# Kernel optimization log

Measured on AMD Instinct MI355X. Metric: run time of the kernel, lower is better.

The kernel has to match this reference:

```python
import jax, jax.numpy as jnp
import numpy as np

B, N, D = 16, 8192, 768
H = int(D * 4.0)  # mlp hidden
EPS = 1e-6
D_SQRT = D ** (-0.5)


def setup_inputs() -> dict:
    key = jax.random.key(0)
    ks = jax.random.split(key, 6)
    x = jax.random.normal(ks[0], (B, N, D), dtype=jnp.float32)
    # learnable query, trunc-normal std = D**-0.5 (plain normal is fine for a reference)
    query = jax.random.normal(ks[1], (D,), dtype=jnp.float32) * D_SQRT
    ln_gamma = jnp.ones((D,), dtype=jnp.float32)
    ln_beta = jnp.zeros((D,), dtype=jnp.float32)
    w1 = jax.random.normal(ks[2], (D, H), dtype=jnp.float32) * (D ** -0.5)
    b1 = jnp.zeros((H,), dtype=jnp.float32)
    w2 = jax.random.normal(ks[3], (H, D), dtype=jnp.float32) * (H ** -0.5)
    b2 = jnp.zeros((D,), dtype=jnp.float32)
    return {"x": x, "query": query, "ln_gamma": ln_gamma, "ln_beta": ln_beta,
            "w1": w1, "b1": b1, "w2": w2, "b2": b2}


def _layernorm(x, gamma, beta):
    mu = jnp.mean(x, axis=-1, keepdims=True)
    var = jnp.mean(jnp.square(x - mu), axis=-1, keepdims=True)
    return (x - mu) * jax.lax.rsqrt(var + EPS) * gamma + beta


def reference(x, query, ln_gamma, ln_beta, w1, b1, w2, b2):
    # single-query cross attention: attn [B, N]
    attn = jnp.einsum('d,bnd->bn', query, x)
    attn_sm = jax.nn.softmax(attn * D_SQRT, axis=-1)
    pooled = jnp.einsum('bn,bnd->bd', attn_sm, x)  # [B, D]
    h = _layernorm(pooled, ln_gamma, ln_beta)
    h = jax.nn.gelu(h @ w1 + b1, approximate=False) @ w2 + b2
    out = pooled + h
    return out, attn
```

## Files before the change

### kernel.cpp

```cpp
#include <hip/hip_runtime.h>
#include <hip/hip_bf16.h>
#include <math.h>

#define BB 16
#define NN 8192
#define DD 768
#define HH 3072
#define EPSV 1e-6f
#define DSQRT 0.03608439182435161f

#define CHUNKS 128
#define ROWS_PER_BLOCK (NN / CHUNKS)
#define NWAVES 4
#define ROWS_PER_WAVE (ROWS_PER_BLOCK / NWAVES)
#define PSTRIDE 772

#define KS1 16
#define KL1 (DD / KS1)
#define KS2 48
#define KL2 (HH / KS2)

__global__ __launch_bounds__(256, 4) void attn_pool_k(
    const float* __restrict__ x, const float* __restrict__ query,
    float* __restrict__ attn_out, float* __restrict__ partials)
{
    const int b     = blockIdx.y;
    const int chunk = blockIdx.x;
    const int tid   = threadIdx.x;
    const int wave  = tid >> 6;
    const int lane  = tid & 63;

    const float4* q4 = (const float4*)query;
    const float4 q0 = q4[lane];
    const float4 q1 = q4[lane + 64];
    const float4 q2 = q4[lane + 128];

    float4 p0 = make_float4(0.f, 0.f, 0.f, 0.f);
    float4 p1 = make_float4(0.f, 0.f, 0.f, 0.f);
    float4 p2 = make_float4(0.f, 0.f, 0.f, 0.f);
    float esum = 0.f;

    const int n0 = chunk * ROWS_PER_BLOCK + wave * ROWS_PER_WAVE;
    const float4* xb = (const float4*)(x + (size_t)b * NN * DD);

    #pragma unroll 2
    for (int r = 0; r < ROWS_PER_WAVE; ++r) {
        const int n = n0 + r;
        const float4* xr = xb + (size_t)n * (DD / 4);
        const float4 v0 = xr[lane];
        const float4 v1 = xr[lane + 64];
        const float4 v2 = xr[lane + 128];

        float s = v0.x * q0.x + v0.y * q0.y + v0.z * q0.z + v0.w * q0.w;
        s += v1.x * q1.x + v1.y * q1.y + v1.z * q1.z + v1.w * q1.w;
        s += v2.x * q2.x + v2.y * q2.y + v2.z * q2.z + v2.w * q2.w;
        #pragma unroll
        for (int off = 32; off > 0; off >>= 1) s += __shfl_xor(s, off);

        if (lane == 0) attn_out[(size_t)b * NN + n] = s;

        const float e = expf(s * DSQRT);
        esum += e;
        p0.x += e * v0.x; p0.y += e * v0.y; p0.z += e * v0.z; p0.w += e * v0.w;
        p1.x += e * v1.x; p1.y += e * v1.y; p1.z += e * v1.z; p1.w += e * v1.w;
        p2.x += e * v2.x; p2.y += e * v2.y; p2.z += e * v2.z; p2.w += e * v2.w;
    }

    __shared__ float lds[NWAVES][PSTRIDE];
    float* my = lds[wave];
    *(float4*)&my[lane * 4]       = p0;
    *(float4*)&my[256 + lane * 4] = p1;
    *(float4*)&my[512 + lane * 4] = p2;
    if (lane == 0) my[768] = esum;
    __syncthreads();

    float* outp = partials + (size_t)(b * CHUNKS + chunk) * PSTRIDE;
    #pragma unroll
    for (int k = 0; k < 3; ++k) {
        const int idx = tid + k * 256;
        outp[idx] = lds[0][idx] + lds[1][idx] + lds[2][idx] + lds[3][idx];
    }
    if (tid == 0) outp[768] = lds[0][768] + lds[1][768] + lds[2][768] + lds[3][768];
}

__global__ __launch_bounds__(768) void reduce_ln_k(
    const float* __restrict__ partials, const float* __restrict__ gamma,
    const float* __restrict__ beta, float* __restrict__ pooled_ws,
    float* __restrict__ hln_ws)
{
    const int b = blockIdx.x, tid = threadIdx.x;
    const float* pb = partials + (size_t)b * CHUNKS * PSTRIDE;

    float v = 0.f;
    #pragma unroll 8
    for (int c = 0; c < CHUNKS; ++c) v += pb[c * PSTRIDE + tid];

    __shared__ float s_den;
    if (tid < 64) {
        float dn = pb[tid * PSTRIDE + 768] + pb[(tid + 64) * PSTRIDE + 768];
        #pragma unroll
        for (int off = 32; off > 0; off >>= 1) dn += __shfl_xor(dn, off);
        if (tid == 0) s_den = dn;
    }
    __syncthreads();
    v *= (1.f / s_den);

    __shared__ float red[768];
    red[tid] = v;
    __syncthreads();
    if (tid < 256) red[tid] += red[tid + 256] + red[tid + 512];
    __syncthreads();
    for (int s = 128; s > 0; s >>= 1) {
        if (tid < s) red[tid] += red[tid + s];
        __syncthreads();
    }
    const float mu = red[0] * (1.f / 768.f);
    __syncthreads();

    const float dmu = v - mu;
    red[tid] = dmu * dmu;
    __syncthreads();
    if (tid < 256) red[tid] += red[tid + 256] + red[tid + 512];
    __syncthreads();
    for (int s = 128; s > 0; s >>= 1) {
        if (tid < s) red[tid] += red[tid + s];
        __syncthreads();
    }
    const float var = red[0] * (1.f / 768.f);
    const float rstd = rsqrtf(var + EPSV);

    pooled_ws[(size_t)b * DD + tid] = v;
    hln_ws[(size_t)b * DD + tid] = (v - mu) * rstd * gamma[tid] + beta[tid];
}

__global__ __launch_bounds__(256) void gemm1_part_k(
    const float* __restrict__ hln_ws, const float* __restrict__ w1,
    float* __restrict__ g1p)
{
    const int j  = blockIdx.x * 256 + threadIdx.x;
    const int k0 = blockIdx.y * KL1;

    __shared__ float hl[BB][KL1];
    for (int i = threadIdx.x; i < BB * KL1; i += 256) {
        const int b = i / KL1, d = i - b * KL1;
        hl[b][d] = hln_ws[(size_t)b * DD + k0 + d];
    }
    __syncthreads();

    float wv[KL1];
    #pragma unroll
    for (int d = 0; d < KL1; ++d) wv[d] = w1[(size_t)(k0 + d) * HH + j];

    float acc[BB];
    #pragma unroll
    for (int b = 0; b < BB; ++b) acc[b] = 0.f;

    #pragma unroll
    for (int d4 = 0; d4 < KL1 / 4; ++d4) {
        #pragma unroll
        for (int b = 0; b < BB; ++b) {
            const float4 h4 = *(const float4*)&hl[b][d4 * 4];
            acc[b] += h4.x * wv[d4 * 4] + h4.y * wv[d4 * 4 + 1]
                    + h4.z * wv[d4 * 4 + 2] + h4.w * wv[d4 * 4 + 3];
        }
    }

    float* op = g1p + (size_t)blockIdx.y * BB * HH;
    #pragma unroll
    for (int b = 0; b < BB; ++b) op[(size_t)b * HH + j] = acc[b];
}

__global__ __launch_bounds__(256) void comb1_gelu_k(
    const float* __restrict__ g1p, const float* __restrict__ b1,
    float* __restrict__ h1_ws)
{
    const int i = blockIdx.x * 256 + threadIdx.x;
    const int j = i % HH;

    float a = b1[j];
    #pragma unroll
    for (int s = 0; s < KS1; ++s) a += g1p[(size_t)s * BB * HH + i];
    h1_ws[i] = 0.5f * a * (1.f + erff(a * 0.70710678118654752f));
}

__global__ __launch_bounds__(256) void gemm2_part_k(
    const float* __restrict__ h1_ws, const float* __restrict__ w2,
    float* __restrict__ g2p)
{
    const int col = blockIdx.x * 256 + threadIdx.x;
    const int k0  = blockIdx.y * KL2;

    __shared__ float hg[BB][KL2];
    for (int i = threadIdx.x; i < BB * KL2; i += 256) {
        const int b = i / KL2, d = i - b * KL2;
        hg[b][d] = h1_ws[(size_t)b * HH + k0 + d];
    }
    __syncthreads();

    float wv[KL2];
    #pragma unroll
    for (int d = 0; d < KL2; ++d) wv[d] = w2[(size_t)(k0 + d) * DD + col];

    float acc[BB];
    #pragma unroll
    for (int b = 0; b < BB; ++b) acc[b] = 0.f;

    #pragma unroll
    for (int d4 = 0; d4 < KL2 / 4; ++d4) {
        #pragma unroll
        for (int b = 0; b < BB; ++b) {
            const float4 h4 = *(const float4*)&hg[b][d4 * 4];
            acc[b] += h4.x * wv[d4 * 4] + h4.y * wv[d4 * 4 + 1]
                    + h4.z * wv[d4 * 4 + 2] + h4.w * wv[d4 * 4 + 3];
        }
    }

    float* op = g2p + (size_t)blockIdx.y * BB * DD;
    #pragma unroll
    for (int b = 0; b < BB; ++b) op[(size_t)b * DD + col] = acc[b];
}

__global__ __launch_bounds__(256) void comb2_fin_k(
    const float* __restrict__ g2p, const float* __restrict__ pooled_ws,
    const float* __restrict__ b2, float* __restrict__ out)
{
    const int i = blockIdx.x * 256 + threadIdx.x;
    const int d = i % DD;

    float a = pooled_ws[i] + b2[d];
    #pragma unroll
    for (int s = 0; s < KS2; ++s) a += g2p[(size_t)s * BB * DD + i];
    out[i] = a;
}

extern "C" void kernel_launch(void* const* d_in, const int* in_sizes, int n_in,
                              void* d_out, int out_size, void* d_ws, size_t ws_size,
                              hipStream_t stream)
{
    const float* x     = (const float*)d_in[0];
    const float* query = (const float*)d_in[1];
    const float* gamma = (const float*)d_in[2];
    const float* beta  = (const float*)d_in[3];
    const float* w1    = (const float*)d_in[4];
    const float* b1    = (const float*)d_in[5];
    const float* w2    = (const float*)d_in[6];
    const float* b2    = (const float*)d_in[7];

    float* out      = (float*)d_out;
    float* attn_out = out + BB * DD;

    float* ws       = (float*)d_ws;
    float* partials = ws;
    float* pooled   = partials + BB * CHUNKS * PSTRIDE;
    float* hln      = pooled + BB * DD;
    float* h1       = hln + BB * DD;
    float* g1p      = h1 + BB * HH;
    float* g2p      = g1p + KS1 * BB * HH;

    attn_pool_k<<<dim3(CHUNKS, BB), 256, 0, stream>>>(x, query, attn_out, partials);
    reduce_ln_k<<<dim3(BB), 768, 0, stream>>>(partials, gamma, beta, pooled, hln);
    gemm1_part_k<<<dim3(HH / 256, KS1), 256, 0, stream>>>(hln, w1, g1p);
    comb1_gelu_k<<<dim3(BB * HH / 256), 256, 0, stream>>>(g1p, b1, h1);
    gemm2_part_k<<<dim3(DD / 256, KS2), 256, 0, stream>>>(h1, w2, g2p);
    comb2_fin_k<<<dim3(BB * DD / 256), 256, 0, stream>>>(g2p, pooled, b2, out);
}
```

Baseline: 119.5 us.

## Halve attention chunks and add parallel two-stage partial reduction

After: 109.6 us. 1.09x faster.

```diff
diff --git a/kernel.cpp b/kernel.cpp
--- a/kernel.cpp
+++ b/kernel.cpp
@@ -9,18 +9,19 @@
 #define EPSV 1e-6f
 #define DSQRT 0.03608439182435161f
 
-#define CHUNKS 128
+#define CHUNKS 64
 #define ROWS_PER_BLOCK (NN / CHUNKS)
 #define NWAVES 4
 #define ROWS_PER_WAVE (ROWS_PER_BLOCK / NWAVES)
 #define PSTRIDE 772
+#define QQ 4
 
 #define KS1 16
 #define KL1 (DD / KS1)
 #define KS2 48
 #define KL2 (HH / KS2)
 
-__global__ __launch_bounds__(256, 4) void attn_pool_k(
+__global__ __launch_bounds__(256) void attn_pool_k(
     const float* __restrict__ x, const float* __restrict__ query,
     float* __restrict__ attn_out, float* __restrict__ partials)
 {
@@ -83,27 +84,45 @@
     if (tid == 0) outp[768] = lds[0][768] + lds[1][768] + lds[2][768] + lds[3][768];
 }
 
+__global__ __launch_bounds__(256) void qreduce_k(
+    const float* __restrict__ partials, float* __restrict__ qsum,
+    float* __restrict__ qden)
+{
+    const int slice = blockIdx.x % 3;
+    const int q     = blockIdx.x / 3;
+    const int b     = blockIdx.y;
+    const int tid   = threadIdx.x;
+    const float* pb = partials + (size_t)b * CHUNKS * PSTRIDE;
+
+    const int col = slice * 256 + tid;
+    float s = 0.f;
+    #pragma unroll
+    for (int c = 0; c < CHUNKS / QQ; ++c)
+        s += pb[(q * (CHUNKS / QQ) + c) * PSTRIDE + col];
+    qsum[(size_t)(b * QQ + q) * DD + col] = s;
+
+    if (slice == 0 && tid < CHUNKS / QQ) {
+        float dn = pb[(q * (CHUNKS / QQ) + tid) * PSTRIDE + 768];
+        #pragma unroll
+        for (int off = 8; off > 0; off >>= 1) dn += __shfl_xor(dn, off, 16);
+        if (tid == 0) qden[b * QQ + q] = dn;
+    }
+}
+
 __global__ __launch_bounds__(768) void reduce_ln_k(
-    const float* __restrict__ partials, const float* __restrict__ gamma,
-    const float* __restrict__ beta, float* __restrict__ pooled_ws,
-    float* __restrict__ hln_ws)
+    const float* __restrict__ qsum, const float* __restrict__ qden,
+    const float* __restrict__ gamma, const float* __restrict__ beta,
+    float* __restrict__ pooled_ws, float* __restrict__ hln_ws)
 {
     const int b = blockIdx.x, tid = threadIdx.x;
-    const float* pb = partials + (size_t)b * CHUNKS * PSTRIDE;
 
     float v = 0.f;
-    #pragma unroll 8
-    for (int c = 0; c < CHUNKS; ++c) v += pb[c * PSTRIDE + tid];
-
-    __shared__ float s_den;
-    if (tid < 64) {
-        float dn = pb[tid * PSTRIDE + 768] + pb[(tid + 64) * PSTRIDE + 768];
-        #pragma unroll
-        for (int off = 32; off > 0; off >>= 1) dn += __shfl_xor(dn, off);
-        if (tid == 0) s_den = dn;
-    }
-    __syncthreads();
-    v *= (1.f / s_den);
+    #pragma unroll
+    for (int q = 0; q < QQ; ++q) v += qsum[(size_t)(b * QQ + q) * DD + tid];
+
+    const float den = qden[b * QQ] + qden[b * QQ + 1]
+                    + qden[b * QQ + 2] + qden[b * QQ + 3];
+    v *= (1.f / den);
 
     __shared__ float red[768];
     red[tid] = v;
@@ -251,14 +270,17 @@
 
     float* ws       = (float*)d_ws;
     float* partials = ws;
-    float* pooled   = partials + BB * CHUNKS * PSTRIDE;
+    float* qsum     = partials + BB * CHUNKS * PSTRIDE;
+    float* qden     = qsum + BB * QQ * DD;
+    float* pooled   = qden + 64;
     float* hln      = pooled + BB * DD;
     float* h1       = hln + BB * DD;
     float* g1p      = h1 + BB * HH;
     float* g2p      = g1p + KS1 * BB * HH;
 
     attn_pool_k<<<dim3(CHUNKS, BB), 256, 0, stream>>>(x, query, attn_out, partials);
-    reduce_ln_k<<<dim3(BB), 768, 0, stream>>>(partials, gamma, beta, pooled, hln);
+    qreduce_k<<<dim3(12, BB), 256, 0, stream>>>(partials, qsum, qden);
+    reduce_ln_k<<<dim3(BB), 768, 0, stream>>>(qsum, qden, gamma, beta, pooled, hln);
     gemm1_part_k<<<dim3(HH / 256, KS1), 256, 0, stream>>>(hln, w1, g1p);
     comb1_gelu_k<<<dim3(BB * HH / 256), 256, 0, stream>>>(g1p, b1, h1);
     gemm2_part_k<<<dim3(DD / 256, KS2), 256, 0, stream>>>(h1, w2, g2p);
```
